# Kernel optimization log

Measured on AMD Instinct MI355X. Metric: run time of the kernel, lower is better.

## Reference

```python
import jax, jax.numpy as jnp
import numpy as np
from jax import lax

IN_CH = 128
INTER_CH = 128
AUDIO_CH = 1
K = 2
DILATIONS = [2 ** i for i in range(10)] * 4  # 40 blocks
B, T = 4, 8192


def _causal_conv1d(x, w, dilation):
    # x: [B, Cin, T], w: [Cout, Cin, K] -> [B, Cout, T], left-padded (causal)
    pad = dilation * (w.shape[-1] - 1)
    return lax.conv_general_dilated(
        x, w, window_strides=(1,), padding=[(pad, 0)],
        rhs_dilation=(dilation,), dimension_numbers=('NCH', 'OIH', 'NCH'))


def setup_inputs() -> dict:
    key = jax.random.key(0)
    ks = jax.random.split(key, 12)
    L = len(DILATIONS)
    s = 0.05
    return {
        'x': jax.random.normal(ks[0], (B, AUDIO_CH, T), jnp.float32),
        'pre_w': jax.random.normal(ks[1], (IN_CH, AUDIO_CH, 3), jnp.float32) * s,
        'pre_b': jax.random.normal(ks[2], (IN_CH,), jnp.float32) * s,
        'conv_w': jax.random.normal(ks[3], (L, 2 * INTER_CH, IN_CH, K), jnp.float32) * s,
        'conv_b': jax.random.normal(ks[4], (L, 2 * INTER_CH), jnp.float32) * s,
        'post_w': jax.random.normal(ks[5], (L, IN_CH, INTER_CH), jnp.float32) * s,
        'post_b': jax.random.normal(ks[6], (L, IN_CH), jnp.float32) * s,
        'lin1_w': jax.random.normal(ks[7], (INTER_CH, INTER_CH), jnp.float32) * s,
        'lin1_b': jax.random.normal(ks[8], (INTER_CH,), jnp.float32) * s,
        'lin2_w': jax.random.normal(ks[9], (IN_CH, INTER_CH), jnp.float32) * s,
        'lin2_b': jax.random.normal(ks[10], (IN_CH,), jnp.float32) * s,
    }


def reference(x, pre_w, pre_b, conv_w, conv_b, post_w, post_b,
              lin1_w, lin1_b, lin2_w, lin2_b):
    # pre_net: ConstantPad1d((2,0)) + Conv1d(k=3) == causal conv, dilation 1
    h = _causal_conv1d(x, pre_w, 1) + pre_b[None, :, None]  # [B, IN_CH, T]
    skip_sum = jnp.zeros((x.shape[0], INTER_CH, x.shape[-1]), h.dtype)
    for i, d in enumerate(DILATIONS):
        y = _causal_conv1d(h, conv_w[i], d) + conv_b[i][None, :, None]  # [B, 2*INTER, T]
        a, b = jnp.split(y, 2, axis=1)
        skip = a * jax.nn.sigmoid(b)                                    # GLU
        h = h + jnp.einsum('oc,bct->bot', post_w[i], skip) + post_b[i][None, :, None]
        skip_sum = skip_sum + skip
    # conv2sa: [B, C, T] -> [T, B, C]
    z = jnp.transpose(skip_sum, (2, 0, 1))
    z = jax.nn.relu(z)
    z = z @ lin1_w.T + lin1_b
    z = jax.nn.relu(z)
    return z @ lin2_w.T + lin2_b  # [T, B, IN_CH]
```

## Files before the change

kernel.cpp:

```cpp
#include <hip/hip_runtime.h>
#include <hip/hip_bf16.h>

typedef __bf16 bf16;
typedef unsigned long long u64;
typedef __bf16 bf16x8 __attribute__((ext_vector_type(8)));
typedef __bf16 bf16x4 __attribute__((ext_vector_type(4)));
typedef float f32x4 __attribute__((ext_vector_type(4)));

#define NB 4
#define T 8192
#define C 128
#define NBLK 40
#define XS 136

#define MFMA(a, b, c) __builtin_amdgcn_mfma_f32_16x16x32_bf16(a, b, c, 0, 0, 0)

__device__ __forceinline__ float bf2f(bf16 x){ return (float)x; }
__device__ __forceinline__ bf16 f2bf(float x){ return (bf16)x; }

__device__ __forceinline__ float ld(const void* p, int i, int isbf){
    return isbf ? bf2f(((const bf16*)p)[i]) : ((const float*)p)[i];
}

__device__ __forceinline__ bf16x4 ld8(const bf16* p){
    u64 v = __hip_atomic_load((const u64*)p, __ATOMIC_RELAXED, __HIP_MEMORY_SCOPE_AGENT);
    return __builtin_bit_cast(bf16x4, v);
}
__device__ __forceinline__ void st16c(bf16* p, f32x4 v){
    asm volatile("global_store_dwordx4 %0, %1, off sc0 sc1" :: "v"(p), "v"(v) : "memory");
}

__global__ __launch_bounds__(64) void k_detect(const unsigned short* __restrict__ u,
                                               int* __restrict__ flag){
    unsigned short v = u[threadIdx.x * 2];
    int e = (v >> 7) & 255;
    bool sane = (e >= 100 && e <= 140) || ((v & 0x7FFF) == 0);
    unsigned long long m = __ballot(sane);
    if (threadIdx.x == 0) *flag = (__popcll(m) >= 48) ? 1 : 0;
}

__global__ __launch_bounds__(256) void k_prep(
    const void* __restrict__ conv_w, const void* __restrict__ post_w,
    const void* __restrict__ lin1_w, const void* __restrict__ lin2_w,
    const void* __restrict__ x,      const void* __restrict__ conv_b,
    const void* __restrict__ post_b, const void* __restrict__ pre_w,
    const void* __restrict__ pre_b,  const void* __restrict__ lin1_b,
    const void* __restrict__ lin2_b,
    bf16* __restrict__ weff, bf16* __restrict__ pwc,
    bf16* __restrict__ w1c,  bf16* __restrict__ w2c,
    float* __restrict__ xc,  float* __restrict__ cbf,
    float* __restrict__ pbf, float* __restrict__ misc,
    const int* __restrict__ flag){
    int f = *flag;
    int g = blockIdx.x * 256 + threadIdx.x;
    if (g < 327680){
        int blk = g >> 13, r = g & 8191, o = r >> 5, j = r & 31;
        int k = (j >= 16) ? 1 : 0;
        int base = blk * 65536 + o * 256 + (j * 8 - k * 128) * 2 + k;
        bf16x8 v;
#pragma unroll
        for (int m = 0; m < 8; m++) v[m] = f2bf(ld(conv_w, base + m * 2, f));
        *(bf16x8*)(weff + (size_t)g * 8) = v;
    } else if (g < 409600){
        int e = (g - 327680) * 8;
        bf16x8 v;
#pragma unroll
        for (int m = 0; m < 8; m++) v[m] = f2bf(ld(post_w, e + m, f));
        *(bf16x8*)(pwc + e) = v;
    } else if (g < 411648){
        int e = (g - 409600) * 8;
        bf16x8 v;
#pragma unroll
        for (int m = 0; m < 8; m++) v[m] = f2bf(ld(lin1_w, e + m, f));
        *(bf16x8*)(w1c + e) = v;
    } else if (g < 413696){
        int e = (g - 411648) * 8;
        bf16x8 v;
#pragma unroll
        for (int m = 0; m < 8; m++) v[m] = f2bf(ld(lin2_w, e + m, f));
        *(bf16x8*)(w2c + e) = v;
    } else if (g < 417792){
        int e = (g - 413696) * 8;
#pragma unroll
        for (int m = 0; m < 8; m++) xc[e + m] = ld(x, e + m, f);
    } else if (g < 419072){
        int e = (g - 417792) * 8;
#pragma unroll
        for (int m = 0; m < 8; m++) cbf[e + m] = ld(conv_b, e + m, f);
    } else if (g < 419712){
        int e = (g - 419072) * 8;
#pragma unroll
        for (int m = 0; m < 8; m++) pbf[e + m] = ld(post_b, e + m, f);
    } else if (g < 419808){
        int e = (g - 419712) * 8;
#pragma unroll
        for (int m = 0; m < 8; m++){
            int idx = e + m;
            if      (idx < 384) misc[idx] = ld(pre_w,  idx,       f);
            else if (idx < 512) misc[idx] = ld(pre_b,  idx - 384, f);
            else if (idx < 640) misc[idx] = ld(lin1_b, idx - 512, f);
            else                misc[idx] = ld(lin2_b, idx - 640, f);
        }
    }
}

__device__ __forceinline__ void wait_ge(unsigned* p, unsigned v){
    int guard = 0;
    while (__hip_atomic_load(p, __ATOMIC_RELAXED, __HIP_MEMORY_SCOPE_AGENT) < v){
        __builtin_amdgcn_s_sleep(1);
        if (++guard > (1 << 22)) break;
    }
    asm volatile("" ::: "memory");
}

__device__ __forceinline__ void tail_store(const bf16* Xo, bf16* dst, int nrows, int tid){
    int ngr = nrows * 16;
    for (int g = tid; g < ngr; g += 512){
        int rr = 128 - nrows + (g >> 4), co = (g & 15) * 8;
        f32x4 v = *(const f32x4*)(Xo + rr * XS + co);
        st16c(dst + (size_t)rr * C + co, v);
    }
    asm volatile("s_waitcnt vmcnt(0)" ::: "memory");
}

__global__ __launch_bounds__(512, 2) void k_main(
    const float* __restrict__ xc,  const float* __restrict__ misc,
    const bf16* __restrict__ weff, const float* __restrict__ cbf,
    const bf16* __restrict__ pwc,  const float* __restrict__ pbf,
    const bf16* __restrict__ w1c,  const bf16* __restrict__ w2c,
    bf16* __restrict__ hA, bf16* __restrict__ hB,
    unsigned* __restrict__ prog, unsigned* __restrict__ cons,
    void* __restrict__ outv, const int* __restrict__ flag)
{
    __shared__ __align__(16) bf16 Xo[128 * XS];
    __shared__ __align__(16) bf16 Xh[128 * XS];

    int tid  = threadIdx.x;
    int wg   = blockIdx.x;
    int b    = wg >> 6;
    int slab = wg & 63;
    int t0   = slab * 128;
    int wv = tid >> 6, ln = tid & 63, lo = ln & 15, quad = ln >> 4;
    const size_t hb = (size_t)b * T * C;

    float hreg[32];
    float ssum[32];

    {
        const float* xr = xc + b * T;
#pragma unroll
        for (int ct = 0; ct < 8; ct++){
            int t = t0 + ct * 16 + lo;
            float x0 = (t >= 2) ? xr[t - 2] : 0.f;
            float x1 = (t >= 1) ? xr[t - 1] : 0.f;
            float x2 = xr[t];
            bf16x4 hv;
#pragma unroll
            for (int r = 0; r < 4; r++){
                int c = wv * 16 + quad * 4 + r;
                float acc = misc[384 + c] + misc[c*3]*x0 + misc[c*3+1]*x1 + misc[c*3+2]*x2;
                hreg[ct * 4 + r] = acc;
                hv[r] = f2bf(acc);
            }
            *(bf16x4*)(Xo + (ct * 16 + lo) * XS + wv * 16 + quad * 4) = hv;
        }
    }
#pragma unroll
    for (int i = 0; i < 32; i++) ssum[i] = 0.f;
    __syncthreads();
    if (slab < 63) tail_store(Xo, hA + hb + (size_t)t0 * C, 1, tid);
    __syncthreads();
    if (tid == 0)
        __hip_atomic_store(prog + wg, 1u, __ATOMIC_RELAXED, __HIP_MEMORY_SCOPE_AGENT);

    for (int i = 0; i < NBLK; i++){
        int d  = 1 << (i % 10);
        int D  = (d >= 128) ? (d >> 7) : 1;
        int dn = (i < NBLK - 1) ? (1 << ((i + 1) % 10)) : 0;
        int Dn = (dn >= 128) ? (dn >> 7) : 1;
        int nst = (dn < 128) ? dn : 128;
        bool last = (i == NBLK - 1);
        bool do_store = !last && (slab + Dn <= 63);
        const bf16* hin  = (i & 1) ? hB : hA;
        bf16*       hout = (i & 1) ? hA : hB;
        const bf16* wb   = weff + ((size_t)i << 16);
        const bf16* pwb  = pwc  + i * 16384;
        const float* cb  = cbf + i * 256;
        const float* pb  = pbf + i * 128;

        f32x4 cacc0[8] = {}, cacc1[8] = {};

#pragma unroll
        for (int kk = 0; kk < 4; kk++){
            int ko = 128 + kk * 32 + quad * 8;
            bf16x8 a0 = *(const bf16x8*)(wb + (size_t)(wv*16 + lo) * 256 + ko);
            bf16x8 a1 = *(const bf16x8*)(wb + (size_t)(128 + wv*16 + lo) * 256 + ko);
#pragma unroll
            for (int ct = 0; ct < 8; ct++){
                bf16x8 bf_ = *(const bf16x8*)(Xo + (ct*16 + lo) * XS + kk*32 + quad*8);
                cacc0[ct] = MFMA(a0, bf_, cacc0[ct]);
                cacc1[ct] = MFMA(a1, bf_, cacc1[ct]);
            }
        }
        if (slab >= D) wait_ge(prog + (wg - D), (unsigned)(i + 1));
        {
            int tbase = t0 - d;
#pragma unroll
            for (int j = 0; j < 8; j++){
                int g = j * 512 + tid;
                int row = g >> 5, c4 = (g & 31) << 2;
                int t = tbase + row;
                bf16x4 v = {};
                if (t >= t0)      v = *(const bf16x4*)(Xo + (t - t0) * XS + c4);
                else if (t >= 0)  v = ld8(hin + hb + (size_t)t * C + c4);
                *(bf16x4*)(Xh + row * XS + c4) = v;
            }
        }
        __syncthreads();
        if (!last && tid == 0)
            __hip_atomic_store(cons + wg, (unsigned)(i + 1),
                               __ATOMIC_RELAXED, __HIP_MEMORY_SCOPE_AGENT);
#pragma unroll
        for (int kk = 0; kk < 4; kk++){
            int ko = kk * 32 + quad * 8;
            bf16x8 a0 = *(const bf16x8*)(wb + (size_t)(wv*16 + lo) * 256 + ko);
            bf16x8 a1 = *(const bf16x8*)(wb + (size_t)(128 + wv*16 + lo) * 256 + ko);
#pragma unroll
            for (int ct = 0; ct < 8; ct++){
                bf16x8 bf_ = *(const bf16x8*)(Xh + (ct*16 + lo) * XS + kk*32 + quad*8);
                cacc0[ct] = MFMA(a0, bf_, cacc0[ct]);
                cacc1[ct] = MFMA(a1, bf_, cacc1[ct]);
            }
        }
        __syncthreads();
#pragma unroll
        for (int ct = 0; ct < 8; ct++){
            int col = ct * 16 + lo;
            bf16x4 sv;
#pragma unroll
            for (int r = 0; r < 4; r++){
                int j = wv * 16 + quad * 4 + r;
                float a = cacc0[ct][r] + cb[j];
                float g = cacc1[ct][r] + cb[128 + j];
                float s = a * __builtin_amdgcn_rcpf(1.f + __expf(-g));
                ssum[ct * 4 + r] += s;
                sv[r] = f2bf(s);
            }
            if (!last) *(bf16x4*)(Xh + col * XS + wv * 16 + quad * 4) = sv;
        }
        if (last) break;
        __syncthreads();
        {
            f32x4 pacc[8] = {};
#pragma unroll
            for (int kk = 0; kk < 4; kk++){
                bf16x8 pa = *(const bf16x8*)(pwb + (wv*16 + lo) * 128 + kk*32 + quad*8);
#pragma unroll
                for (int ct = 0; ct < 8; ct++){
                    bf16x8 pbv = *(const bf16x8*)(Xh + (ct*16 + lo) * XS + kk*32 + quad*8);
                    pacc[ct] = MFMA(pa, pbv, pacc[ct]);
                }
            }
#pragma unroll
            for (int ct = 0; ct < 8; ct++){
                bf16x4 hv;
#pragma unroll
                for (int r = 0; r < 4; r++){
                    hreg[ct * 4 + r] += pacc[ct][r] + pb[wv * 16 + quad * 4 + r];
                    hv[r] = f2bf(hreg[ct * 4 + r]);
                }
                *(bf16x4*)(Xo + (ct * 16 + lo) * XS + wv * 16 + quad * 4) = hv;
            }
        }
        if (do_store && i >= 1){
            int dp = 1 << ((i - 1) % 10);
            int Dp = (dp >= 128) ? (dp >> 7) : 1;
            if (slab + Dp <= 63) wait_ge(cons + (wg + Dp), (unsigned)i);
        }
        __syncthreads();
        if (do_store) tail_store(Xo, hout + hb + (size_t)t0 * C, nst, tid);
        __syncthreads();
        if (tid == 0)
            __hip_atomic_store(prog + wg, (unsigned)(i + 2),
                               __ATOMIC_RELAXED, __HIP_MEMORY_SCOPE_AGENT);
    }

    const float* b1 = misc + 512;
    const float* b2 = misc + 640;
    int isbf = *flag;
    __syncthreads();
#pragma unroll
    for (int ct = 0; ct < 8; ct++){
        int col = ct * 16 + lo;
        bf16x4 zv;
#pragma unroll
        for (int r = 0; r < 4; r++){
            float z = ssum[ct * 4 + r];
            zv[r] = f2bf(z > 0.f ? z : 0.f);
        }
        *(bf16x4*)(Xh + col * XS + wv * 16 + quad * 4) = zv;
    }
    __syncthreads();
    f32x4 a1[8] = {};
#pragma unroll
    for (int kk = 0; kk < 4; kk++){
        bf16x8 pa = *(const bf16x8*)(w1c + (wv*16 + lo) * 128 + kk*32 + quad*8);
#pragma unroll
        for (int ct = 0; ct < 8; ct++){
            bf16x8 pbv = *(const bf16x8*)(Xh + (ct*16 + lo) * XS + kk*32 + quad*8);
            a1[ct] = MFMA(pa, pbv, a1[ct]);
        }
    }
    __syncthreads();
#pragma unroll
    for (int ct = 0; ct < 8; ct++){
        int col = ct * 16 + lo;
        bf16x4 uv;
#pragma unroll
        for (int r = 0; r < 4; r++){
            int row = wv * 16 + quad * 4 + r;
            float u = a1[ct][r] + b1[row];
            uv[r] = f2bf(u > 0.f ? u : 0.f);
        }
        *(bf16x4*)(Xh + col * XS + wv * 16 + quad * 4) = uv;
    }
    __syncthreads();
    f32x4 a2[8] = {};
#pragma unroll
    for (int kk = 0; kk < 4; kk++){
        bf16x8 pa = *(const bf16x8*)(w2c + (wv*16 + lo) * 128 + kk*32 + quad*8);
#pragma unroll
        for (int ct = 0; ct < 8; ct++){
            bf16x8 pbv = *(const bf16x8*)(Xh + (ct*16 + lo) * XS + kk*32 + quad*8);
            a2[ct] = MFMA(pa, pbv, a2[ct]);
        }
    }
#pragma unroll
    for (int ct = 0; ct < 8; ct++){
        int col = t0 + ct * 16 + lo;
#pragma unroll
        for (int r = 0; r < 4; r++){
            int row = wv * 16 + quad * 4 + r;
            float v = a2[ct][r] + b2[row];
            size_t oi = ((size_t)col * NB + b) * C + row;
            if (isbf) ((bf16*)outv)[oi] = f2bf(v);
            else      ((float*)outv)[oi] = v;
        }
    }
}

extern "C" void kernel_launch(void* const* d_in, const int* in_sizes, int n_in,
                              void* d_out, int out_size, void* d_ws, size_t ws_size,
                              hipStream_t stream){
    const void* x      = d_in[0];
    const void* pre_w  = d_in[1];
    const void* pre_b  = d_in[2];
    const void* conv_w = d_in[3];
    const void* conv_b = d_in[4];
    const void* post_w = d_in[5];
    const void* post_b = d_in[6];
    const void* lin1w  = d_in[7];
    const void* lin1b  = d_in[8];
    const void* lin2w  = d_in[9];
    const void* lin2b  = d_in[10];

    char* ws = (char*)d_ws;
    bf16*     hA   = (bf16*)    (ws);
    bf16*     hB   = (bf16*)    (ws +  8388608);
    bf16*     weff = (bf16*)    (ws + 16777216);
    bf16*     pwc  = (bf16*)    (ws + 22020096);
    bf16*     w1c  = (bf16*)    (ws + 23330816);
    bf16*     w2c  = (bf16*)    (ws + 23363584);
    float*    xc   = (float*)   (ws + 23396352);
    float*    cbf  = (float*)   (ws + 23527424);
    float*    pbf  = (float*)   (ws + 23568384);
    float*    misc = (float*)   (ws + 23588864);
    int*      flag = (int*)     (ws + 23591936);
    unsigned* prog = (unsigned*)(ws + 23592960);
    unsigned* cons = (unsigned*)(ws + 23593984);

    hipMemsetAsync(prog, 0, 2048, stream);
    k_detect<<<1, 64, 0, stream>>>((const unsigned short*)x, flag);
    k_prep<<<1640, 256, 0, stream>>>(conv_w, post_w, lin1w, lin2w, x, conv_b,
                                     post_b, pre_w, pre_b, lin1b, lin2b,
                                     weff, pwc, w1c, w2c, xc, cbf, pbf, misc, flag);

    const float* xc_c   = xc;   const float* misc_c = misc;
    const bf16*  weff_c = weff; const float* cbf_c  = cbf;
    const bf16*  pwc_c  = pwc;  const float* pbf_c  = pbf;
    const bf16*  w1c_c  = w1c;  const bf16*  w2c_c  = w2c;
    void* out_v = d_out;        const int* flag_c = flag;
    void* ka[14] = { &xc_c, &misc_c, &weff_c, &cbf_c, &pwc_c, &pbf_c,
                     &w1c_c, &w2c_c, &hA, &hB, &prog, &cons, &out_v, &flag_c };
    hipLaunchCooperativeKernel((void*)k_main, dim3(256), dim3(512), ka, 0, stream);
}
```

Measured before the change: 545.8 us.

## Fuse first six dilation layers per cycle using a 64-row halo to cut inter-slab sync

Each 10-layer cycle now loads a 64-row halo from the left neighbour once, then computes dilations 1 through 32 locally on a 192-row LDS tile, recomputing the halo rows redundantly. Global stores, progress flags and neighbour waits now happen only at cycle entry and for the four large-dilation layers, instead of after every layer. This trades about 50% extra MFMA work on the first six layers, plus larger LDS buffers that may reduce occupancy, for far fewer cross-workgroup synchronisations and global round-trips.

Measured after the change: 586.2 us. +7.4%, slower.

```diff
diff --git a/kernel.cpp b/kernel.cpp
--- a/kernel.cpp
+++ b/kernel.cpp
@@ -113,11 +113,11 @@
     asm volatile("" ::: "memory");
 }
 
-__device__ __forceinline__ void tail_store(const bf16* Xo, bf16* dst, int nrows, int tid){
-    int ngr = nrows * 16;
+__device__ __forceinline__ void tail_store192(const bf16* Xo, bf16* dst, int nst, int tid){
+    int ngr = nst * 16;
     for (int g = tid; g < ngr; g += 512){
-        int rr = 128 - nrows + (g >> 4), co = (g & 15) * 8;
-        f32x4 v = *(const f32x4*)(Xo + rr * XS + co);
+        int rr = 128 - nst + (g >> 4), co = (g & 15) * 8;
+        f32x4 v = *(const f32x4*)(Xo + (64 + rr) * XS + co);
         st16c(dst + (size_t)rr * C + co, v);
     }
     asm volatile("s_waitcnt vmcnt(0)" ::: "memory");
@@ -132,8 +132,9 @@
     unsigned* __restrict__ prog, unsigned* __restrict__ cons,
     void* __restrict__ outv, const int* __restrict__ flag)
 {
-    __shared__ __align__(16) bf16 Xo[128 * XS];
-    __shared__ __align__(16) bf16 Xh[128 * XS];
+    __shared__ __align__(16) bf16 XoA[192 * XS];
+    __shared__ __align__(16) bf16 XoB[192 * XS];
+    bf16* Xh = XoB;
 
     int tid  = threadIdx.x;
     int wg   = blockIdx.x;
@@ -162,127 +163,251 @@
                 hreg[ct * 4 + r] = acc;
                 hv[r] = f2bf(acc);
             }
-            *(bf16x4*)(Xo + (ct * 16 + lo) * XS + wv * 16 + quad * 4) = hv;
+            *(bf16x4*)(XoA + (64 + ct * 16 + lo) * XS + wv * 16 + quad * 4) = hv;
         }
     }
 #pragma unroll
     for (int i = 0; i < 32; i++) ssum[i] = 0.f;
     __syncthreads();
-    if (slab < 63) tail_store(Xo, hA + hb + (size_t)t0 * C, 1, tid);
+    if (slab < 63) tail_store192(XoA, hB + hb + (size_t)t0 * C, 64, tid);
     __syncthreads();
     if (tid == 0)
         __hip_atomic_store(prog + wg, 1u, __ATOMIC_RELAXED, __HIP_MEMORY_SCOPE_AGENT);
 
-    for (int i = 0; i < NBLK; i++){
-        int d  = 1 << (i % 10);
-        int D  = (d >= 128) ? (d >> 7) : 1;
-        int dn = (i < NBLK - 1) ? (1 << ((i + 1) % 10)) : 0;
-        int Dn = (dn >= 128) ? (dn >> 7) : 1;
-        int nst = (dn < 128) ? dn : 128;
-        bool last = (i == NBLK - 1);
-        bool do_store = !last && (slab + Dn <= 63);
-        const bf16* hin  = (i & 1) ? hB : hA;
-        bf16*       hout = (i & 1) ? hA : hB;
-        const bf16* wb   = weff + ((size_t)i << 16);
-        const bf16* pwb  = pwc  + i * 16384;
-        const float* cb  = cbf + i * 256;
-        const float* pb  = pbf + i * 128;
-
-        f32x4 cacc0[8] = {}, cacc1[8] = {};
-
-#pragma unroll
-        for (int kk = 0; kk < 4; kk++){
-            int ko = 128 + kk * 32 + quad * 8;
-            bf16x8 a0 = *(const bf16x8*)(wb + (size_t)(wv*16 + lo) * 256 + ko);
-            bf16x8 a1 = *(const bf16x8*)(wb + (size_t)(128 + wv*16 + lo) * 256 + ko);
+    for (int c = 0; c < 4; c++){
+        const int ib = 10 * c;
+
+        {
+            float hregH[16];
+            const int k_entry = 5 * c + 1;
+            const bf16* hEnt = (k_entry & 1) ? hB : hA;
+            if (slab >= 1) wait_ge(prog + (wg - 1), (unsigned)k_entry);
+            {
+                int tbase = t0 - 64;
+#pragma unroll
+                for (int jj = 0; jj < 4; jj++){
+                    int g = jj * 512 + tid;
+                    int row = g >> 5, c4 = (g & 31) << 2;
+                    int t = tbase + row;
+                    bf16x4 v = {};
+                    if (t >= 0) v = ld8(hEnt + hb + (size_t)t * C + c4);
+                    *(bf16x4*)(XoA + row * XS + c4) = v;
+                }
+            }
+            __syncthreads();
+            if (tid == 0)
+                __hip_atomic_store(cons + wg, (unsigned)k_entry,
+                                   __ATOMIC_RELAXED, __HIP_MEMORY_SCOPE_AGENT);
+#pragma unroll
+            for (int ct = 0; ct < 4; ct++){
+                bf16x4 hv = *(const bf16x4*)(XoA + (ct*16 + lo) * XS + wv*16 + quad*4);
+#pragma unroll
+                for (int r = 0; r < 4; r++) hregH[ct * 4 + r] = bf2f(hv[r]);
+            }
+
+            for (int l = 0; l < 6; l++){
+                const int d = 1 << l;
+                bf16* Xc = (l & 1) ? XoB : XoA;
+                bf16* Xn = (l & 1) ? XoA : XoB;
+                const bf16* wb  = weff + ((size_t)(ib + l) << 16);
+                const bf16* pwb = pwc + (ib + l) * 16384;
+                const float* cb = cbf + (ib + l) * 256;
+                const float* pb = pbf + (ib + l) * 128;
+
+                f32x4 cacc0[12] = {}, cacc1[12] = {};
+#pragma unroll
+                for (int kk = 0; kk < 4; kk++){
+                    int ko = kk * 32 + quad * 8;
+                    bf16x8 a0d = *(const bf16x8*)(wb + (size_t)(wv*16 + lo) * 256 + ko);
+                    bf16x8 a1d = *(const bf16x8*)(wb + (size_t)(128 + wv*16 + lo) * 256 + ko);
+                    bf16x8 a0t = *(const bf16x8*)(wb + (size_t)(wv*16 + lo) * 256 + 128 + ko);
+                    bf16x8 a1t = *(const bf16x8*)(wb + (size_t)(128 + wv*16 + lo) * 256 + 128 + ko);
+#pragma unroll
+                    for (int ct = 0; ct < 12; ct++){
+                        int rt = ct * 16 + lo;
+                        int rd = rt - d; rd = (rd < 0) ? 0 : rd;
+                        bf16x8 bt = *(const bf16x8*)(Xc + rt * XS + ko);
+                        bf16x8 bd = *(const bf16x8*)(Xc + rd * XS + ko);
+                        cacc0[ct] = MFMA(a0d, bd, cacc0[ct]);
+                        cacc0[ct] = MFMA(a0t, bt, cacc0[ct]);
+                        cacc1[ct] = MFMA(a1d, bd, cacc1[ct]);
+                        cacc1[ct] = MFMA(a1t, bt, cacc1[ct]);
+                    }
+                }
+#pragma unroll
+                for (int ct = 0; ct < 12; ct++){
+                    bf16x4 sv;
+#pragma unroll
+                    for (int r = 0; r < 4; r++){
+                        int j = wv * 16 + quad * 4 + r;
+                        float a = cacc0[ct][r] + cb[j];
+                        float g = cacc1[ct][r] + cb[128 + j];
+                        float s = a * __builtin_amdgcn_rcpf(1.f + __expf(-g));
+                        if (ct >= 4) ssum[(ct - 4) * 4 + r] += s;
+                        sv[r] = f2bf(s);
+                    }
+                    *(bf16x4*)(Xn + (ct * 16 + lo) * XS + wv * 16 + quad * 4) = sv;
+                }
+                __syncthreads();
+                f32x4 pacc[12] = {};
+#pragma unroll
+                for (int kk = 0; kk < 4; kk++){
+                    bf16x8 pa = *(const bf16x8*)(pwb + (wv*16 + lo) * 128 + kk*32 + quad*8);
+#pragma unroll
+                    for (int ct = 0; ct < 12; ct++){
+                        bf16x8 pbv = *(const bf16x8*)(Xn + (ct*16 + lo) * XS + kk*32 + quad*8);
+                        pacc[ct] = MFMA(pa, pbv, pacc[ct]);
+                    }
+                }
+                __syncthreads();
+#pragma unroll
+                for (int ct = 0; ct < 12; ct++){
+                    bf16x4 hv;
+                    if (ct < 4){
+#pragma unroll
+                        for (int r = 0; r < 4; r++){
+                            hregH[ct * 4 + r] += pacc[ct][r] + pb[wv*16 + quad*4 + r];
+                            hv[r] = f2bf(hregH[ct * 4 + r]);
+                        }
+                        if (slab == 0){ bf16x4 z = {}; hv = z; }
+                    } else {
+#pragma unroll
+                        for (int r = 0; r < 4; r++){
+                            hreg[(ct - 4) * 4 + r] += pacc[ct][r] + pb[wv*16 + quad*4 + r];
+                            hv[r] = f2bf(hreg[(ct - 4) * 4 + r]);
+                        }
+                    }
+                    *(bf16x4*)(Xn + (ct * 16 + lo) * XS + wv * 16 + quad * 4) = hv;
+                }
+                __syncthreads();
+            }
+            {
+                const int k_st = 5 * c + 2;
+                bool stg = (slab + 1 <= 63);
+                if (stg){
+                    if (c >= 1 && slab + 4 <= 63)
+                        wait_ge(cons + (wg + 4), (unsigned)(5 * c));
+                    tail_store192(XoA, ((k_st & 1) ? hB : hA) + hb + (size_t)t0 * C, 64, tid);
+                }
+                __syncthreads();
+                if (tid == 0)
+                    __hip_atomic_store(prog + wg, (unsigned)k_st,
+                                       __ATOMIC_RELAXED, __HIP_MEMORY_SCOPE_AGENT);
+            }
+        }
+
+        for (int j = 6; j <= 9; j++){
+            const int i = ib + j;
+            const int d = 64 << (j - 6);
+            const int D = (j <= 7) ? 1 : ((j == 8) ? 2 : 4);
+            const int k_cons = 5 * c + (j - 4);
+            const int k_st   = k_cons + 1;
+            const int nst    = (j == 9) ? 64 : 128;
+            const bool last  = (i == NBLK - 1);
+            const int Dr_st  = (j == 6) ? 1 : ((j == 7) ? 2 : ((j == 8) ? 4 : 1));
+            const bool do_store = !last && (slab + Dr_st <= 63);
+            const int kow    = k_st - 2;
+            const int Dr_ow  = (j == 9) ? 2 : 1;
+            const bf16* hin  = (k_cons & 1) ? hB : hA;
+            bf16*       hout = (k_st & 1) ? hB : hA;
+            const bf16* wb   = weff + ((size_t)i << 16);
+            const bf16* pwb  = pwc  + i * 16384;
+            const float* cb  = cbf + i * 256;
+            const float* pb  = pbf + i * 128;
+
+            f32x4 cacc0[8] = {}, cacc1[8] = {};
+#pragma unroll
+            for (int kk = 0; kk < 4; kk++){
+                int ko = 128 + kk * 32 + quad * 8;
+                bf16x8 a0 = *(const bf16x8*)(wb + (size_t)(wv*16 + lo) * 256 + ko);
+                bf16x8 a1 = *(const bf16x8*)(wb + (size_t)(128 + wv*16 + lo) * 256 + ko);
+#pragma unroll
+                for (int ct = 0; ct < 8; ct++){
+                    bf16x8 bf_ = *(const bf16x8*)(XoA + (64 + ct*16 + lo) * XS + kk*32 + quad*8);
+                    cacc0[ct] = MFMA(a0, bf_, cacc0[ct]);
+                    cacc1[ct] = MFMA(a1, bf_, cacc1[ct]);
+                }
+            }
+            if (slab >= D) wait_ge(prog + (wg - D), (unsigned)k_cons);
+            {
+                int tbase = t0 - d;
+#pragma unroll
+                for (int jj = 0; jj < 8; jj++){
+                    int g = jj * 512 + tid;
+                    int row = g >> 5, c4 = (g & 31) << 2;
+                    int t = tbase + row;
+                    bf16x4 v = {};
+                    if (t >= t0)      v = *(const bf16x4*)(XoA + (64 + t - t0) * XS + c4);
+                    else if (t >= 0)  v = ld8(hin + hb + (size_t)t * C + c4);
+                    *(bf16x4*)(Xh + row * XS + c4) = v;
+                }
+            }
+            __syncthreads();
+            if (!last && tid == 0)
+                __hip_atomic_store(cons + wg, (unsigned)k_cons,
+                                   __ATOMIC_RELAXED, __HIP_MEMORY_SCOPE_AGENT);
+#pragma unroll
+            for (int kk = 0; kk < 4; kk++){
+                int ko = kk * 32 + quad * 8;
+                bf16x8 a0 = *(const bf16x8*)(wb + (size_t)(wv*16 + lo) * 256 + ko);
+                bf16x8 a1 = *(const bf16x8*)(wb + (size_t)(128 + wv*16 + lo) * 256 + ko);
+#pragma unroll
+                for (int ct = 0; ct < 8; ct++){
+                    bf16x8 bf_ = *(const bf16x8*)(Xh + (ct*16 + lo) * XS + kk*32 + quad*8);
+                    cacc0[ct] = MFMA(a0, bf_, cacc0[ct]);
+                    cacc1[ct] = MFMA(a1, bf_, cacc1[ct]);
+                }
+            }
+            __syncthreads();
 #pragma unroll
             for (int ct = 0; ct < 8; ct++){
-                bf16x8 bf_ = *(const bf16x8*)(Xo + (ct*16 + lo) * XS + kk*32 + quad*8);
-                cacc0[ct] = MFMA(a0, bf_, cacc0[ct]);
-                cacc1[ct] = MFMA(a1, bf_, cacc1[ct]);
-            }
-        }
-        if (slab >= D) wait_ge(prog + (wg - D), (unsigned)(i + 1));
-        {
-            int tbase = t0 - d;
-#pragma unroll
-            for (int j = 0; j < 8; j++){
-                int g = j * 512 + tid;
-                int row = g >> 5, c4 = (g & 31) << 2;
-                int t = tbase + row;
-                bf16x4 v = {};
-                if (t >= t0)      v = *(const bf16x4*)(Xo + (t - t0) * XS + c4);
-                else if (t >= 0)  v = ld8(hin + hb + (size_t)t * C + c4);
-                *(bf16x4*)(Xh + row * XS + c4) = v;
-            }
-        }
-        __syncthreads();
-        if (!last && tid == 0)
-            __hip_atomic_store(cons + wg, (unsigned)(i + 1),
-                               __ATOMIC_RELAXED, __HIP_MEMORY_SCOPE_AGENT);
-#pragma unroll
-        for (int kk = 0; kk < 4; kk++){
-            int ko = kk * 32 + quad * 8;
-            bf16x8 a0 = *(const bf16x8*)(wb + (size_t)(wv*16 + lo) * 256 + ko);
-            bf16x8 a1 = *(const bf16x8*)(wb + (size_t)(128 + wv*16 + lo) * 256 + ko);
-#pragma unroll
-            for (int ct = 0; ct < 8; ct++){
-                bf16x8 bf_ = *(const bf16x8*)(Xh + (ct*16 + lo) * XS + kk*32 + quad*8);
-                cacc0[ct] = MFMA(a0, bf_, cacc0[ct]);
-                cacc1[ct] = MFMA(a1, bf_, cacc1[ct]);
-            }
-        }
-        __syncthreads();
-#pragma unroll
-        for (int ct = 0; ct < 8; ct++){
-            int col = ct * 16 + lo;
-            bf16x4 sv;
-#pragma unroll
-            for (int r = 0; r < 4; r++){
-                int j = wv * 16 + quad * 4 + r;
-                float a = cacc0[ct][r] + cb[j];
-                float g = cacc1[ct][r] + cb[128 + j];
-                float s = a * __builtin_amdgcn_rcpf(1.f + __expf(-g));
-                ssum[ct * 4 + r] += s;
-                sv[r] = f2bf(s);
-            }
-            if (!last) *(bf16x4*)(Xh + col * XS + wv * 16 + quad * 4) = sv;
-        }
-        if (last) break;
-        __syncthreads();
-        {
-            f32x4 pacc[8] = {};
-#pragma unroll
-            for (int kk = 0; kk < 4; kk++){
-                bf16x8 pa = *(const bf16x8*)(pwb + (wv*16 + lo) * 128 + kk*32 + quad*8);
+                bf16x4 sv;
+#pragma unroll
+                for (int r = 0; r < 4; r++){
+                    int jj = wv * 16 + quad * 4 + r;
+                    float a = cacc0[ct][r] + cb[jj];
+                    float g = cacc1[ct][r] + cb[128 + jj];
+                    float s = a * __builtin_amdgcn_rcpf(1.f + __expf(-g));
+                    ssum[ct * 4 + r] += s;
+                    sv[r] = f2bf(s);
+                }
+                if (!last) *(bf16x4*)(Xh + (ct*16 + lo) * XS + wv*16 + quad*4) = sv;
+            }
+            if (last) break;
+            __syncthreads();
+            {
+                f32x4 pacc[8] = {};
+#pragma unroll
+                for (int kk = 0; kk < 4; kk++){
+                    bf16x8 pa = *(const bf16x8*)(pwb + (wv*16 + lo) * 128 + kk*32 + quad*8);
+#pragma unroll
+                    for (int ct = 0; ct < 8; ct++){
+                        bf16x8 pbv = *(const bf16x8*)(Xh + (ct*16 + lo) * XS + kk*32 + quad*8);
+                        pacc[ct] = MFMA(pa, pbv, pacc[ct]);
+                    }
+                }
 #pragma unroll
                 for (int ct = 0; ct < 8; ct++){
-                    bf16x8 pbv = *(const bf16x8*)(Xh + (ct*16 + lo) * XS + kk*32 + quad*8);
-                    pacc[ct] = MFMA(pa, pbv, pacc[ct]);
-                }
-            }
-#pragma unroll
-            for (int ct = 0; ct < 8; ct++){
-                bf16x4 hv;
-#pragma unroll
-                for (int r = 0; r < 4; r++){
-                    hreg[ct * 4 + r] += pacc[ct][r] + pb[wv * 16 + quad * 4 + r];
-                    hv[r] = f2bf(hreg[ct * 4 + r]);
-                }
-                *(bf16x4*)(Xo + (ct * 16 + lo) * XS + wv * 16 + quad * 4) = hv;
-            }
-        }
-        if (do_store && i >= 1){
-            int dp = 1 << ((i - 1) % 10);
-            int Dp = (dp >= 128) ? (dp >> 7) : 1;
-            if (slab + Dp <= 63) wait_ge(cons + (wg + Dp), (unsigned)i);
-        }
-        __syncthreads();
-        if (do_store) tail_store(Xo, hout + hb + (size_t)t0 * C, nst, tid);
-        __syncthreads();
-        if (tid == 0)
-            __hip_atomic_store(prog + wg, (unsigned)(i + 2),
-                               __ATOMIC_RELAXED, __HIP_MEMORY_SCOPE_AGENT);
+                    bf16x4 hv;
+#pragma unroll
+                    for (int r = 0; r < 4; r++){
+                        hreg[ct * 4 + r] += pacc[ct][r] + pb[wv*16 + quad*4 + r];
+                        hv[r] = f2bf(hreg[ct * 4 + r]);
+                    }
+                    *(bf16x4*)(XoA + (64 + ct*16 + lo) * XS + wv*16 + quad*4) = hv;
+                }
+            }
+            if (do_store && slab + Dr_ow <= 63)
+                wait_ge(cons + (wg + Dr_ow), (unsigned)kow);
+            if (j == 6 && c >= 1 && do_store && slab + 2 <= 63)
+                wait_ge(cons + (wg + 2), (unsigned)(5 * c - 1));
+            __syncthreads();
+            if (do_store) tail_store192(XoA, hout + hb + (size_t)t0 * C, nst, tid);
+            __syncthreads();
+            if (tid == 0)
+                __hip_atomic_store(prog + wg, (unsigned)k_st,
+                                   __ATOMIC_RELAXED, __HIP_MEMORY_SCOPE_AGENT);
+        }
     }
 
     const float* b1 = misc + 512;
@@ -291,14 +416,13 @@
     __syncthreads();
 #pragma unroll
     for (int ct = 0; ct < 8; ct++){
-        int col = ct * 16 + lo;
         bf16x4 zv;
 #pragma unroll
         for (int r = 0; r < 4; r++){
             float z = ssum[ct * 4 + r];
             zv[r] = f2bf(z > 0.f ? z : 0.f);
         }
-        *(bf16x4*)(Xh + col * XS + wv * 16 + quad * 4) = zv;
+        *(bf16x4*)(Xh + (ct*16 + lo) * XS + wv*16 + quad*4) = zv;
     }
     __syncthreads();
     f32x4 a1[8] = {};
@@ -314,7 +438,6 @@
     __syncthreads();
 #pragma unroll
     for (int ct = 0; ct < 8; ct++){
-        int col = ct * 16 + lo;
         bf16x4 uv;
 #pragma unroll
         for (int r = 0; r < 4; r++){
@@ -322,7 +445,7 @@
             float u = a1[ct][r] + b1[row];
             uv[r] = f2bf(u > 0.f ? u : 0.f);
         }
-        *(bf16x4*)(Xh + col * XS + wv * 16 + quad * 4) = uv;
+        *(bf16x4*)(Xh + (ct*16 + lo) * XS + wv*16 + quad*4) = uv;
     }
     __syncthreads();
     f32x4 a2[8] = {};
```
